# Performance work log

Measured on AMD Instinct MI355X. Metric: run time of the kernel, lower is better.

## Reference

```python
import jax, jax.numpy as jnp
import numpy as np

N_NODES = 100000
N_EDGES = 1600000
IN, HID, OUT = 512, 128, 64


def setup_inputs() -> dict:
    key = jax.random.key(0)
    ks = jax.random.split(key, 7)
    x = jax.random.normal(ks[0], (N_NODES, IN), dtype=jnp.float32)
    rows = jax.random.randint(ks[1], (N_EDGES,), 0, N_NODES, dtype=jnp.int32)
    cols = jax.random.randint(ks[2], (N_EDGES,), 0, N_NODES, dtype=jnp.int32)
    vals = jax.random.uniform(ks[3], (N_EDGES,), dtype=jnp.float32)
    # torch.nn.Linear weights have shape (out_features, in_features)
    W0 = jax.random.normal(ks[4], (HID, IN), dtype=jnp.float32) * (IN ** -0.5)
    W1 = jax.random.normal(ks[5], (HID, HID), dtype=jnp.float32) * (HID ** -0.5)
    W2 = jax.random.normal(ks[6], (OUT, HID), dtype=jnp.float32) * (HID ** -0.5)
    return {"x": x, "rows": rows, "cols": cols, "vals": vals,
            "W0": W0, "W1": W1, "W2": W2}


def reference(x, rows, cols, vals, W0, W1, W2):
    n = x.shape[0]

    def spmm(h):  # out[r] = sum_e vals[e] * h[cols[e]] for rows[e] == r
        return jax.ops.segment_sum(vals[:, None] * h[cols], rows, num_segments=n)

    # layer 0: Linear -> SpMM -> ReLU (dropout p=0.0 is identity)
    h = jax.nn.relu(spmm(x @ W0.T))
    # layer 1
    h = jax.nn.relu(spmm(h @ W1.T))
    # output layer: Linear -> SpMM (no activation)
    return spmm(h @ W2.T)
```

## Files before the change

kernel.cpp:

```cpp
#include <hip/hip_runtime.h>
#include <hip/hip_bf16.h>
#include <cstddef>


typedef unsigned short ushort_t;
typedef unsigned char u8;
using frag_t = __attribute__((ext_vector_type(8))) short;
using accf4 = __attribute__((ext_vector_type(4))) float;

__device__ __forceinline__ ushort_t f2bf(float f) {
    unsigned int u = __float_as_uint(f);
    u += 0x7FFF + ((u >> 16) & 1);
    return (ushort_t)(u >> 16);
}
__device__ __forceinline__ float bf2f(unsigned int u16) {
    return __uint_as_float(u16 << 16);
}
__device__ __forceinline__ u8 f2fp8(float a) {
    return (u8)(__builtin_amdgcn_cvt_pk_fp8_f32(a, 0.f, 0, false) & 0xff);
}
__device__ __forceinline__ void acc4_fp8(float* acc, unsigned q, float v) {
    auto p0 = __builtin_amdgcn_cvt_pk_f32_fp8((int)q, false);
    auto p1 = __builtin_amdgcn_cvt_pk_f32_fp8((int)q, true);
    acc[0] += v * p0[0]; acc[1] += v * p0[1];
    acc[2] += v * p1[0]; acc[3] += v * p1[1];
}
__device__ __forceinline__ void acc8_fp8(float* acc, uint2 q, float v) {
    acc4_fp8(acc, q.x, v);
    acc4_fp8(acc + 4, q.y, v);
}


__global__ __launch_bounds__(256) void init0_k(int* __restrict__ cnt8, int m8,
                                               const float* __restrict__ W1,
                                               const float* __restrict__ W2,
                                               ushort_t* __restrict__ Wb1,
                                               ushort_t* __restrict__ Wb2) {
    int i = blockIdx.x * 256 + threadIdx.x;
    if (i < m8) cnt8[i] = 0;
    if (i < 16384) Wb1[i] = f2bf(W1[i]);
    else if (i < 24576) Wb2[i - 16384] = f2bf(W2[i - 16384]);
}


__device__ void gemm0_body(int bx, const float* __restrict__ A,
                           const float* __restrict__ W, u8* __restrict__ C,
                           int M) {
    constexpr int K = 512, N = 128, BM = 128, BN = 128, BK = 64;
    constexpr int WM = BM / 2, WN = BN / 2;
    constexpr int TI = WM / 16, TJ = WN / 16;
    constexpr int LDA = BK + 8;
    constexpr int T = K / BK;
    constexpr int A_PER = BM * BK / 4 / 256;
    constexpr int B_PER = BN * BK / 4 / 256;

    __shared__ __align__(16) ushort_t As[BM][LDA];
    __shared__ __align__(16) ushort_t Bs[BN][LDA];

    const int tid = threadIdx.x;
    const int lane = tid & 63;
    const int wid = tid >> 6;
    const int wm = wid >> 1, wn = wid & 1;
    const int rowBase = bx * BM;
    const int lrow = lane & 15, kq = lane >> 4;

    float4 aF[A_PER], bF[B_PER];

    auto loadTile = [&](int k0) {
#pragma unroll
        for (int i = 0; i < A_PER; i++) {
            int idx = tid + i * 256;
            int r = idx / (BK / 4), c4 = idx % (BK / 4);
            int grow = rowBase + r;
            aF[i] = (grow < M) ? *(const float4*)(A + (size_t)grow * K + k0 + c4 * 4)
                               : make_float4(0.f, 0.f, 0.f, 0.f);
        }
#pragma unroll
        for (int i = 0; i < B_PER; i++) {
            int idx = tid + i * 256;
            int r = idx / (BK / 4), c4 = idx % (BK / 4);
            bF[i] = *(const float4*)(W + (size_t)r * K + k0 + c4 * 4);
        }
    };
    auto storeTile = [&]() {
#pragma unroll
        for (int i = 0; i < A_PER; i++) {
            int idx = tid + i * 256;
            int r = idx / (BK / 4), c4 = idx % (BK / 4);
            ushort_t p[4] = {f2bf(aF[i].x), f2bf(aF[i].y), f2bf(aF[i].z), f2bf(aF[i].w)};
            *(uint2*)&As[r][c4 * 4] = *(uint2*)p;
        }
#pragma unroll
        for (int i = 0; i < B_PER; i++) {
            int idx = tid + i * 256;
            int r = idx / (BK / 4), c4 = idx % (BK / 4);
            ushort_t p[4] = {f2bf(bF[i].x), f2bf(bF[i].y), f2bf(bF[i].z), f2bf(bF[i].w)};
            *(uint2*)&Bs[r][c4 * 4] = *(uint2*)p;
        }
    };

    accf4 acc[TI][TJ];
#pragma unroll
    for (int i = 0; i < TI; i++)
#pragma unroll
        for (int j = 0; j < TJ; j++) acc[i][j] = accf4{0.f, 0.f, 0.f, 0.f};

    loadTile(0);
    storeTile();
    __syncthreads();

    for (int t = 0; t < T; t++) {
        if (t + 1 < T) loadTile((t + 1) * BK);
#pragma unroll
        for (int ks = 0; ks < BK / 32; ks++) {
            const int kb = ks * 32 + kq * 8;
            frag_t a[TI], b[TJ];
#pragma unroll
            for (int i = 0; i < TI; i++)
                a[i] = *(const frag_t*)&As[wm * WM + i * 16 + lrow][kb];
#pragma unroll
            for (int j = 0; j < TJ; j++)
                b[j] = *(const frag_t*)&Bs[wn * WN + j * 16 + lrow][kb];
#pragma unroll
            for (int i = 0; i < TI; i++)
#pragma unroll
                for (int j = 0; j < TJ; j++)
                    acc[i][j] = __builtin_amdgcn_mfma_f32_16x16x32_bf16(
                        a[i], b[j], acc[i][j], 0, 0, 0);
        }
        __syncthreads();
        if (t + 1 < T) {
            storeTile();
            __syncthreads();
        }
    }

#pragma unroll
    for (int i = 0; i < TI; i++) {
#pragma unroll
        for (int j = 0; j < TJ; j++) {
            int col = wn * WN + j * 16 + lrow;
#pragma unroll
            for (int r = 0; r < 4; r++) {
                int grow = rowBase + wm * WM + i * 16 + kq * 4 + r;
                if (grow < M) C[(size_t)grow * N + col] = f2fp8(acc[i][j][r]);
            }
        }
    }
}

__global__ __launch_bounds__(256) void d2_k(const float* __restrict__ x,
                                            const float* __restrict__ W0,
                                            u8* __restrict__ g0, int M,
                                            const int* __restrict__ rows,
                                            int* __restrict__ cnt8,
                                            int* __restrict__ rank,
                                            int n, int ne, int gblocks) {
    if ((int)blockIdx.x < gblocks) {
        gemm0_body(blockIdx.x, x, W0, g0, M);
    } else {
        int e = ((int)blockIdx.x - gblocks) * 256 + threadIdx.x;
        if (e < ne) {
            int s = blockIdx.x & 7;
            rank[e] = atomicAdd(&cnt8[s * n + rows[e]], 1);
        }
    }
}


__global__ __launch_bounds__(256) void block_totals_t(const int* __restrict__ cnt8,
                                                      int* __restrict__ bsums,
                                                      int n, int m8) {
    __shared__ int s[256];
    int t = threadIdx.x;
    int i = blockIdx.x * 256 + t;
    s[t] = (i < m8) ? cnt8[(i & 7) * n + (i >> 3)] : 0;
    __syncthreads();
    for (int off = 128; off > 0; off >>= 1) {
        if (t < off) s[t] += s[t + off];
        __syncthreads();
    }
    if (t == 0) bsums[blockIdx.x] = s[0];
}

__global__ __launch_bounds__(1024) void scan_mid(int* bsums, int nb) {
    __shared__ int s[1024];
    int t = threadIdx.x;
    int base = t * 4;
    int v0 = (base + 0 < nb) ? bsums[base + 0] : 0;
    int v1 = (base + 1 < nb) ? bsums[base + 1] : 0;
    int v2 = (base + 2 < nb) ? bsums[base + 2] : 0;
    int v3 = (base + 3 < nb) ? bsums[base + 3] : 0;
    int l0 = v0, l1 = l0 + v1, l2 = l1 + v2, l3 = l2 + v3;
    s[t] = l3;
    __syncthreads();
    for (int off = 1; off < 1024; off *= 2) {
        int u = (t >= off) ? s[t - off] : 0;
        __syncthreads();
        s[t] += u;
        __syncthreads();
    }
    int excl = s[t] - l3;
    if (base + 0 < nb) bsums[base + 0] = excl;
    if (base + 1 < nb) bsums[base + 1] = excl + l0;
    if (base + 2 < nb) bsums[base + 2] = excl + l1;
    if (base + 3 < nb) bsums[base + 3] = excl + l2;
}

__global__ __launch_bounds__(256) void scan_final(const int* __restrict__ cnt8,
                                                  const int* __restrict__ offs,
                                                  int* __restrict__ dstbase,
                                                  int* __restrict__ row_ptr,
                                                  int n, int ne, int m8) {
    __shared__ int s[256];
    int t = threadIdx.x;
    int i = blockIdx.x * 256 + t;
    int v = (i < m8) ? cnt8[(i & 7) * n + (i >> 3)] : 0;
    s[t] = v;
    __syncthreads();
    for (int off = 1; off < 256; off *= 2) {
        int u = (t >= off) ? s[t - off] : 0;
        __syncthreads();
        s[t] += u;
        __syncthreads();
    }
    int excl = s[t] - v + offs[blockIdx.x];
    if (i < m8) {
        dstbase[i] = excl;
        if ((i & 7) == 0) row_ptr[i >> 3] = excl;
    }
    if (i == 0) row_ptr[n] = ne;
}


__global__ __launch_bounds__(256) void scatter8_k(const int* __restrict__ rows,
                                                  const int* __restrict__ cols,
                                                  const float* __restrict__ vals,
                                                  const int* __restrict__ dstbase,
                                                  const int* __restrict__ rank,
                                                  unsigned* __restrict__ es,
                                                  int ne, int gblocks) {
    int e = blockIdx.x * 256 + threadIdx.x;
    if (e >= ne) return;
    int s = (gblocks + (int)blockIdx.x) & 7;
    int r = rows[e];
    int p = dstbase[r * 8 + s] + rank[e];
    es[p] = ((unsigned)cols[e] << 14) | ((unsigned)f2bf(vals[e]) & 0x3fff);
}


__device__ __forceinline__ void gather_pair_128(const int* __restrict__ row_ptr,
                                                const unsigned* __restrict__ es,
                                                const u8* __restrict__ Gp,
                                                int rowA, int rowB, int n,
                                                int g, float* accA, float* accB) {
    int sA = 0, eA = 0, sB = 0, eB = 0;
    if (rowA < n) { sA = row_ptr[rowA]; eA = row_ptr[rowA + 1]; }
    if (rowB < n) { sB = row_ptr[rowB]; eB = row_ptr[rowB + 1]; }
    int nbA = (eA - sA + 15) >> 4, nbB = (eB - sB + 15) >> 4;
    int nb = nbA > nbB ? nbA : nbB;
    for (int b = 0; b < nb; b++) {
        unsigned edA[4], edB[4];
#pragma unroll
        for (int u = 0; u < 4; u++) {
            int ia = sA + b * 16 + u * 4 + g;
            edA[u] = (ia < eA) ? es[ia] : 0u;
        }
#pragma unroll
        for (int u = 0; u < 4; u++) {
            int ib = sB + b * 16 + u * 4 + g;
            edB[u] = (ib < eB) ? es[ib] : 0u;
        }
        uint2 qA[4], qB[4];
#pragma unroll
        for (int u = 0; u < 4; u++) {
            qA[u] = make_uint2(0, 0);
            if (edA[u] & 0x3fff) qA[u] = *(const uint2*)(Gp + (size_t)(edA[u] >> 14) * 128);
        }
#pragma unroll
        for (int u = 0; u < 4; u++) {
            qB[u] = make_uint2(0, 0);
            if (edB[u] & 0x3fff) qB[u] = *(const uint2*)(Gp + (size_t)(edB[u] >> 14) * 128);
        }
#pragma unroll
        for (int u = 0; u < 4; u++) acc8_fp8(accA, qA[u], bf2f(edA[u] & 0x3fff));
#pragma unroll
        for (int u = 0; u < 4; u++) acc8_fp8(accB, qB[u], bf2f(edB[u] & 0x3fff));
    }
}

template <int NOUT>
__global__ __launch_bounds__(256) void spmm_mfma(const int* __restrict__ row_ptr,
                                                 const unsigned* __restrict__ es,
                                                 const u8* __restrict__ G,
                                                 const ushort_t* __restrict__ Wb,
                                                 u8* __restrict__ Hout, int n) {
    constexpr int TJ = NOUT / 64;
    constexpr int SEG = NOUT / 16;

    __shared__ __align__(16) ushort_t Hs[16][136];
    __shared__ __align__(16) u8 Os[16][NOUT + 16];

    const int tid = threadIdx.x;
    const int lane = tid & 63;
    const int wid = tid >> 6;
    const int g = lane >> 4, lg = lane & 15;
    const int lrow = lane & 15, kq = lane >> 4;
    const int rowBase = blockIdx.x * 16;

    const u8* __restrict__ Gp = G + lg * 8;
#pragma unroll
    for (int pr = 0; pr < 2; pr++) {
        int rowA = rowBase + wid * 4 + pr * 2;
        int rowB = rowA + 1;
        float accA[8], accB[8];
#pragma unroll
        for (int k = 0; k < 8; k++) { accA[k] = 0.f; accB[k] = 0.f; }
        gather_pair_128(row_ptr, es, Gp, rowA, rowB, n, g, accA, accB);
#pragma unroll
        for (int k = 0; k < 8; k++) {
            accA[k] += __shfl_xor(accA[k], 16);
            accA[k] += __shfl_xor(accA[k], 32);
            accB[k] += __shfl_xor(accB[k], 16);
            accB[k] += __shfl_xor(accB[k], 32);
        }
        if (g == 0) {
            uint4 o;
            o.x = (unsigned)f2bf(fmaxf(accA[0], 0.f)) | ((unsigned)f2bf(fmaxf(accA[1], 0.f)) << 16);
            o.y = (unsigned)f2bf(fmaxf(accA[2], 0.f)) | ((unsigned)f2bf(fmaxf(accA[3], 0.f)) << 16);
            o.z = (unsigned)f2bf(fmaxf(accA[4], 0.f)) | ((unsigned)f2bf(fmaxf(accA[5], 0.f)) << 16);
            o.w = (unsigned)f2bf(fmaxf(accA[6], 0.f)) | ((unsigned)f2bf(fmaxf(accA[7], 0.f)) << 16);
            *(uint4*)&Hs[wid * 4 + pr * 2][lg * 8] = o;
        }
        if (g == 1) {
            uint4 o;
            o.x = (unsigned)f2bf(fmaxf(accB[0], 0.f)) | ((unsigned)f2bf(fmaxf(accB[1], 0.f)) << 16);
            o.y = (unsigned)f2bf(fmaxf(accB[2], 0.f)) | ((unsigned)f2bf(fmaxf(accB[3], 0.f)) << 16);
            o.z = (unsigned)f2bf(fmaxf(accB[4], 0.f)) | ((unsigned)f2bf(fmaxf(accB[5], 0.f)) << 16);
            o.w = (unsigned)f2bf(fmaxf(accB[6], 0.f)) | ((unsigned)f2bf(fmaxf(accB[7], 0.f)) << 16);
            *(uint4*)&Hs[wid * 4 + pr * 2 + 1][lg * 8] = o;
        }
    }

    frag_t bfr[4][TJ];
#pragma unroll
    for (int ks = 0; ks < 4; ks++)
#pragma unroll
        for (int j = 0; j < TJ; j++)
            bfr[ks][j] = *(const frag_t*)&Wb[(size_t)(wid * 16 * TJ + j * 16 + lrow) * 128 +
                                             ks * 32 + kq * 8];
    __syncthreads();

    accf4 oacc[TJ];
#pragma unroll
    for (int j = 0; j < TJ; j++) oacc[j] = accf4{0.f, 0.f, 0.f, 0.f};
#pragma unroll
    for (int ks = 0; ks < 4; ks++) {
        frag_t a = *(const frag_t*)&Hs[lrow][ks * 32 + kq * 8];
#pragma unroll
        for (int j = 0; j < TJ; j++)
            oacc[j] = __builtin_amdgcn_mfma_f32_16x16x32_bf16(a, bfr[ks][j], oacc[j], 0, 0, 0);
    }
#pragma unroll
    for (int j = 0; j < TJ; j++) {
        int col = wid * 16 * TJ + j * 16 + lrow;
#pragma unroll
        for (int r = 0; r < 4; r++) Os[kq * 4 + r][col] = f2fp8(oacc[j][r]);
    }
    __syncthreads();

    if (tid < 16 * SEG) {
        int row16 = tid / SEG, sg = tid % SEG;
        if (rowBase + row16 < n)
            *(uint4*)&Hout[(size_t)(rowBase + row16) * NOUT + sg * 16] =
                *(const uint4*)&Os[row16][sg * 16];
    }
}


__global__ __launch_bounds__(256) void spmm_csr_64f(const int* __restrict__ row_ptr,
                                                    const unsigned* __restrict__ es,
                                                    const u8* __restrict__ G,
                                                    float* __restrict__ H, int n) {
    const int lane = threadIdx.x & 63;
    const int wid = threadIdx.x >> 6;
    const int g = lane >> 4, lg = lane & 15;
    const int rowA = blockIdx.x * 8 + wid * 2;
    const int rowB = rowA + 1;

    int sA = 0, eA = 0, sB = 0, eB = 0;
    if (rowA < n) { sA = row_ptr[rowA]; eA = row_ptr[rowA + 1]; }
    if (rowB < n) { sB = row_ptr[rowB]; eB = row_ptr[rowB + 1]; }
    int nbA = (eA - sA + 15) >> 4, nbB = (eB - sB + 15) >> 4;
    int nb = nbA > nbB ? nbA : nbB;

    float accA[4] = {0.f, 0.f, 0.f, 0.f}, accB[4] = {0.f, 0.f, 0.f, 0.f};
    const u8* __restrict__ Gp = G + lg * 4;
    for (int b = 0; b < nb; b++) {
        unsigned edA[4], edB[4];
#pragma unroll
        for (int u = 0; u < 4; u++) {
            int ia = sA + b * 16 + u * 4 + g;
            edA[u] = (ia < eA) ? es[ia] : 0u;
        }
#pragma unroll
        for (int u = 0; u < 4; u++) {
            int ib = sB + b * 16 + u * 4 + g;
            edB[u] = (ib < eB) ? es[ib] : 0u;
        }
        unsigned qA[4], qB[4];
#pragma unroll
        for (int u = 0; u < 4; u++) {
            qA[u] = 0;
            if (edA[u] & 0x3fff) qA[u] = *(const unsigned*)(Gp + (size_t)(edA[u] >> 14) * 64);
        }
#pragma unroll
        for (int u = 0; u < 4; u++) {
            qB[u] = 0;
            if (edB[u] & 0x3fff) qB[u] = *(const unsigned*)(Gp + (size_t)(edB[u] >> 14) * 64);
        }
#pragma unroll
        for (int u = 0; u < 4; u++) acc4_fp8(accA, qA[u], bf2f(edA[u] & 0x3fff));
#pragma unroll
        for (int u = 0; u < 4; u++) acc4_fp8(accB, qB[u], bf2f(edB[u] & 0x3fff));
    }
#pragma unroll
    for (int k = 0; k < 4; k++) {
        accA[k] += __shfl_xor(accA[k], 16);
        accA[k] += __shfl_xor(accA[k], 32);
        accB[k] += __shfl_xor(accB[k], 16);
        accB[k] += __shfl_xor(accB[k], 32);
    }
    if (g == 0 && rowA < n) {
        float4 o = make_float4(accA[0], accA[1], accA[2], accA[3]);
        *(float4*)(H + (size_t)rowA * 64 + lg * 4) = o;
    }
    if (g == 1 && rowB < n) {
        float4 o = make_float4(accB[0], accB[1], accB[2], accB[3]);
        *(float4*)(H + (size_t)rowB * 64 + lg * 4) = o;
    }
}

static inline size_t align_up(size_t x, size_t a) { return (x + a - 1) & ~(a - 1); }

extern "C" void kernel_launch(void* const* d_in, const int* in_sizes, int n_in,
                              void* d_out, int out_size, void* d_ws, size_t ws_size,
                              hipStream_t stream) {
    const float* x = (const float*)d_in[0];
    const int* rows = (const int*)d_in[1];
    const int* cols = (const int*)d_in[2];
    const float* vals = (const float*)d_in[3];
    const float* W0 = (const float*)d_in[4];
    const float* W1 = (const float*)d_in[5];
    const float* W2 = (const float*)d_in[6];
    float* out = (float*)d_out;

    const int IN = 512, HID = 128, OUT = 64;
    const int n = in_sizes[0] / IN;
    const int ne = in_sizes[1];
    (void)OUT;

    char* ws = (char*)d_ws;
    size_t off = 0;
    u8* g0 = (u8*)(ws + off); off = align_up(off + (size_t)n * HID, 512);
    u8* g1 = (u8*)(ws + off); off = align_up(off + (size_t)n * HID, 512);
    u8* g2 = (u8*)(ws + off); off = align_up(off + (size_t)n * 64, 512);
    unsigned* es2 = (unsigned*)(ws + off); off = align_up(off + (size_t)ne * 4, 512);
    int* cnt8 = (int*)(ws + off); off = align_up(off + (size_t)8 * n * 4, 512);
    int* rank = (int*)(ws + off); off = align_up(off + (size_t)ne * 4, 512);
    int* dstbase = (int*)(ws + off); off = align_up(off + (size_t)8 * n * 4, 512);
    int* row_ptr = (int*)(ws + off); off = align_up(off + (size_t)(n + 1) * 4, 512);
    int* bsum0 = (int*)(ws + off); off = align_up(off + 4096 * 4, 512);
    ushort_t* Wb1 = (ushort_t*)(ws + off); off = align_up(off + (size_t)HID * HID * 2, 512);
    ushort_t* Wb2 = (ushort_t*)(ws + off); off = align_up(off + (size_t)64 * HID * 2, 512);

    const int eb = (ne + 255) / 256;
    const int m8 = 8 * n;
    const int nb8 = (m8 + 255) / 256;
    const int gblocks = (n + 127) / 128;
    const int fblocks = (n + 15) / 16;

    init0_k<<<nb8, 256, 0, stream>>>(cnt8, m8, W1, W2, Wb1, Wb2);

    d2_k<<<gblocks + eb, 256, 0, stream>>>(x, W0, g0, n, rows, cnt8, rank,
                                           n, ne, gblocks);

    block_totals_t<<<nb8, 256, 0, stream>>>(cnt8, bsum0, n, m8);
    scan_mid<<<1, 1024, 0, stream>>>(bsum0, nb8);
    scan_final<<<nb8, 256, 0, stream>>>(cnt8, bsum0, dstbase, row_ptr, n, ne, m8);
    scatter8_k<<<eb, 256, 0, stream>>>(rows, cols, vals, dstbase, rank, es2,
                                       ne, gblocks);

    spmm_mfma<128><<<fblocks, 256, 0, stream>>>(row_ptr, es2, g0, Wb1, g1, n);
    spmm_mfma<64><<<fblocks, 256, 0, stream>>>(row_ptr, es2, g1, Wb2, g2, n);
    spmm_csr_64f<<<(n + 7) / 8, 256, 0, stream>>>(row_ptr, es2, g2, out, n);
}
```

Measured before the change: 547.8 us.

## Split fused GEMM/histogram kernel and prefetch next edge block in SpMM loops

The combined kernel that ran the layer-0 GEMM blocks and the edge-histogram atomics in one launch is split into two separate kernels launched back to back. The slot index in the scatter kernel is adjusted to match the new histogram block numbering. The CSR gather loops in the SpMM paths now load the next 16-edge block's packed entries while the current block's feature gathers run, so index-load latency overlaps with compute. The split gives up concurrent execution of the GEMM and the atomics, and prefetching adds register pressure.

```diff
diff --git a/kernel.cpp b/kernel.cpp
--- a/kernel.cpp
+++ b/kernel.cpp
@@ -43,9 +43,9 @@
 }
 
 
-__device__ void gemm0_body(int bx, const float* __restrict__ A,
-                           const float* __restrict__ W, u8* __restrict__ C,
-                           int M) {
+__global__ __launch_bounds__(256) void gemm0_k(const float* __restrict__ A,
+                                               const float* __restrict__ W,
+                                               u8* __restrict__ C, int M) {
     constexpr int K = 512, N = 128, BM = 128, BN = 128, BK = 64;
     constexpr int WM = BM / 2, WN = BN / 2;
     constexpr int TI = WM / 16, TJ = WN / 16;
@@ -61,7 +61,7 @@
     const int lane = tid & 63;
     const int wid = tid >> 6;
     const int wm = wid >> 1, wn = wid & 1;
-    const int rowBase = bx * BM;
+    const int rowBase = blockIdx.x * BM;
     const int lrow = lane & 15, kq = lane >> 4;
 
     float4 aF[A_PER], bF[B_PER];
@@ -149,22 +149,15 @@
     }
 }
 
-__global__ __launch_bounds__(256) void d2_k(const float* __restrict__ x,
-                                            const float* __restrict__ W0,
-                                            u8* __restrict__ g0, int M,
-                                            const int* __restrict__ rows,
-                                            int* __restrict__ cnt8,
-                                            int* __restrict__ rank,
-                                            int n, int ne, int gblocks) {
-    if ((int)blockIdx.x < gblocks) {
-        gemm0_body(blockIdx.x, x, W0, g0, M);
-    } else {
-        int e = ((int)blockIdx.x - gblocks) * 256 + threadIdx.x;
-        if (e < ne) {
-            int s = blockIdx.x & 7;
-            rank[e] = atomicAdd(&cnt8[s * n + rows[e]], 1);
-        }
-    }
+
+__global__ __launch_bounds__(256) void hist8_k(const int* __restrict__ rows,
+                                               int* __restrict__ cnt8,
+                                               int* __restrict__ rank,
+                                               int n, int ne) {
+    int e = blockIdx.x * 256 + threadIdx.x;
+    if (e >= ne) return;
+    int s = blockIdx.x & 7;
+    rank[e] = atomicAdd(&cnt8[s * n + rows[e]], 1);
 }
 
 
@@ -238,11 +231,10 @@
                                                   const float* __restrict__ vals,
                                                   const int* __restrict__ dstbase,
                                                   const int* __restrict__ rank,
-                                                  unsigned* __restrict__ es,
-                                                  int ne, int gblocks) {
+                                                  unsigned* __restrict__ es, int ne) {
     int e = blockIdx.x * 256 + threadIdx.x;
     if (e >= ne) return;
-    int s = (gblocks + (int)blockIdx.x) & 7;
+    int s = blockIdx.x & 7;
     int r = rows[e];
     int p = dstbase[r * 8 + s] + rank[e];
     es[p] = ((unsigned)cols[e] << 14) | ((unsigned)f2bf(vals[e]) & 0x3fff);
@@ -259,17 +251,25 @@
     if (rowB < n) { sB = row_ptr[rowB]; eB = row_ptr[rowB + 1]; }
     int nbA = (eA - sA + 15) >> 4, nbB = (eB - sB + 15) >> 4;
     int nb = nbA > nbB ? nbA : nbB;
+    if (nb <= 0) return;
+
+    unsigned edA[4], edB[4], nxA[4], nxB[4];
+#pragma unroll
+    for (int u = 0; u < 4; u++) {
+        int ia = sA + u * 4 + g;
+        edA[u] = (ia < eA) ? es[ia] : 0u;
+        int ib = sB + u * 4 + g;
+        edB[u] = (ib < eB) ? es[ib] : 0u;
+    }
     for (int b = 0; b < nb; b++) {
-        unsigned edA[4], edB[4];
-#pragma unroll
-        for (int u = 0; u < 4; u++) {
-            int ia = sA + b * 16 + u * 4 + g;
-            edA[u] = (ia < eA) ? es[ia] : 0u;
-        }
-#pragma unroll
-        for (int u = 0; u < 4; u++) {
-            int ib = sB + b * 16 + u * 4 + g;
-            edB[u] = (ib < eB) ? es[ib] : 0u;
+        if (b + 1 < nb) {
+#pragma unroll
+            for (int u = 0; u < 4; u++) {
+                int ia = sA + (b + 1) * 16 + u * 4 + g;
+                nxA[u] = (ia < eA) ? es[ia] : 0u;
+                int ib = sB + (b + 1) * 16 + u * 4 + g;
+                nxB[u] = (ib < eB) ? es[ib] : 0u;
+            }
         }
         uint2 qA[4], qB[4];
 #pragma unroll
@@ -286,6 +286,8 @@
         for (int u = 0; u < 4; u++) acc8_fp8(accA, qA[u], bf2f(edA[u] & 0x3fff));
 #pragma unroll
         for (int u = 0; u < 4; u++) acc8_fp8(accB, qB[u], bf2f(edB[u] & 0x3fff));
+#pragma unroll
+        for (int u = 0; u < 4; u++) { edA[u] = nxA[u]; edB[u] = nxB[u]; }
     }
 }
 
@@ -396,33 +398,44 @@
 
     float accA[4] = {0.f, 0.f, 0.f, 0.f}, accB[4] = {0.f, 0.f, 0.f, 0.f};
     const u8* __restrict__ Gp = G + lg * 4;
-    for (int b = 0; b < nb; b++) {
-        unsigned edA[4], edB[4];
+
+    if (nb > 0) {
+        unsigned edA[4], edB[4], nxA[4], nxB[4];
 #pragma unroll
         for (int u = 0; u < 4; u++) {
-            int ia = sA + b * 16 + u * 4 + g;
+            int ia = sA + u * 4 + g;
             edA[u] = (ia < eA) ? es[ia] : 0u;
-        }
-#pragma unroll
-        for (int u = 0; u < 4; u++) {
-            int ib = sB + b * 16 + u * 4 + g;
+            int ib = sB + u * 4 + g;
             edB[u] = (ib < eB) ? es[ib] : 0u;
         }
-        unsigned qA[4], qB[4];
-#pragma unroll
-        for (int u = 0; u < 4; u++) {
-            qA[u] = 0;
-            if (edA[u] & 0x3fff) qA[u] = *(const unsigned*)(Gp + (size_t)(edA[u] >> 14) * 64);
-        }
-#pragma unroll
-        for (int u = 0; u < 4; u++) {
-            qB[u] = 0;
-            if (edB[u] & 0x3fff) qB[u] = *(const unsigned*)(Gp + (size_t)(edB[u] >> 14) * 64);
-        }
-#pragma unroll
-        for (int u = 0; u < 4; u++) acc4_fp8(accA, qA[u], bf2f(edA[u] & 0x3fff));
-#pragma unroll
-        for (int u = 0; u < 4; u++) acc4_fp8(accB, qB[u], bf2f(edB[u] & 0x3fff));
+        for (int b = 0; b < nb; b++) {
+            if (b + 1 < nb) {
+#pragma unroll
+                for (int u = 0; u < 4; u++) {
+                    int ia = sA + (b + 1) * 16 + u * 4 + g;
+                    nxA[u] = (ia < eA) ? es[ia] : 0u;
+                    int ib = sB + (b + 1) * 16 + u * 4 + g;
+                    nxB[u] = (ib < eB) ? es[ib] : 0u;
+                }
+            }
+            unsigned qA[4], qB[4];
+#pragma unroll
+            for (int u = 0; u < 4; u++) {
+                qA[u] = 0;
+                if (edA[u] & 0x3fff) qA[u] = *(const unsigned*)(Gp + (size_t)(edA[u] >> 14) * 64);
+            }
+#pragma unroll
+            for (int u = 0; u < 4; u++) {
+                qB[u] = 0;
+                if (edB[u] & 0x3fff) qB[u] = *(const unsigned*)(Gp + (size_t)(edB[u] >> 14) * 64);
+            }
+#pragma unroll
+            for (int u = 0; u < 4; u++) acc4_fp8(accA, qA[u], bf2f(edA[u] & 0x3fff));
+#pragma unroll
+            for (int u = 0; u < 4; u++) acc4_fp8(accB, qB[u], bf2f(edB[u] & 0x3fff));
+#pragma unroll
+            for (int u = 0; u < 4; u++) { edA[u] = nxA[u]; edB[u] = nxB[u]; }
+        }
     }
 #pragma unroll
     for (int k = 0; k < 4; k++) {
@@ -482,14 +495,14 @@
 
     init0_k<<<nb8, 256, 0, stream>>>(cnt8, m8, W1, W2, Wb1, Wb2);
 
-    d2_k<<<gblocks + eb, 256, 0, stream>>>(x, W0, g0, n, rows, cnt8, rank,
-                                           n, ne, gblocks);
+    hist8_k<<<eb, 256, 0, stream>>>(rows, cnt8, rank, n, ne);
+
+    gemm0_k<<<gblocks, 256, 0, stream>>>(x, W0, g0, n);
 
     block_totals_t<<<nb8, 256, 0, stream>>>(cnt8, bsum0, n, m8);
     scan_mid<<<1, 1024, 0, stream>>>(bsum0, nb8);
     scan_final<<<nb8, 256, 0, stream>>>(cnt8, bsum0, dstbase, row_ptr, n, ne, m8);
-    scatter8_k<<<eb, 256, 0, stream>>>(rows, cols, vals, dstbase, rank, es2,
-                                       ne, gblocks);
+    scatter8_k<<<eb, 256, 0, stream>>>(rows, cols, vals, dstbase, rank, es2, ne);
 
     spmm_mfma<128><<<fblocks, 256, 0, stream>>>(row_ptr, es2, g0, Wb1, g1, n);
     spmm_mfma<64><<<fblocks, 256, 0, stream>>>(row_ptr, es2, g1, Wb2, g2, n);
```

After: 583.9 us. +6.6%, slower.
